# Performance work log

Measured on AMD Instinct MI355X. Metric: run time of the kernel, lower is better.

## Reference

```python
import jax, jax.numpy as jnp
import numpy as np

NUM_EXPERTS = 8
TOP_K = 2
N_EMBD = 1024
D_FFN = 2048  # 4*n_embd//top_k, already multiple of block_size=128


def setup_inputs() -> dict:
    key = jax.random.key(0)
    k1, k2, k3, k4 = jax.random.split(key, 4)
    x = jax.random.normal(k1, (4, 2048, N_EMBD), dtype=jnp.float32)
    router_w = jax.random.normal(k2, (NUM_EXPERTS, N_EMBD), dtype=jnp.float32) * 0.02
    w1 = jax.random.normal(k3, (N_EMBD, D_FFN * NUM_EXPERTS), dtype=jnp.float32) * 0.02
    w2 = jax.random.normal(k4, (D_FFN * NUM_EXPERTS, N_EMBD), dtype=jnp.float32) * 0.02
    return {"x": x, "router_w": router_w, "w1": w1, "w2": w2}


def reference(x, router_w, w1, w2):
    B, T, D = x.shape
    xf = x.reshape(B * T, D)                       # [N, d]
    N = B * T

    # Router: softmax over experts, then top-k selection and renormalization.
    logits = xf @ router_w.T                       # [N, E]
    probs = jax.nn.softmax(logits, axis=-1)
    top_v, top_i = jax.lax.top_k(probs, TOP_K)     # [N, k]
    top_v = top_v / jnp.sum(top_v, axis=-1, keepdims=True)  # norm_topk_prob=True

    # Dense [N, E] routing-weight matrix (zero for non-selected experts).
    gate = jnp.zeros((N, NUM_EXPERTS), dtype=x.dtype)
    gate = gate.at[jnp.arange(N)[:, None], top_i].set(top_v)

    w1r = w1.reshape(D, NUM_EXPERTS, D_FFN)        # expert-major column blocks
    w2r = w2.reshape(NUM_EXPERTS, D_FFN, D)

    out = jnp.zeros((N, D), dtype=x.dtype)
    for e in range(NUM_EXPERTS):
        h = jax.nn.gelu(xf @ w1r[:, e, :], approximate=False)  # [N, f]
        out = out + gate[:, e:e + 1] * (h @ w2r[e])
    return out.reshape(B, T, D)
```

## Files before the change

kernel.cpp:

```cpp
#include <hip/hip_runtime.h>
#include <hip/hip_bf16.h>
#include <cstdint>
#include <cstddef>

#define NE 8
#define N_TOK 8192
#define D_EMB 1024
#define D_FFN 2048

#define BM 128
#define BN 128
#define BK 32

typedef __attribute__((ext_vector_type(8))) short short8;
typedef __attribute__((ext_vector_type(4))) float f32x4;

__device__ __forceinline__ unsigned short f2bf(float f) {
  union { float f; unsigned int u; } c; c.f = f;
  unsigned int u = c.u;
  unsigned int r = u + 0x7FFFu + ((u >> 16) & 1u);
  return (unsigned short)(r >> 16);
}

__device__ __forceinline__ float bf2f(unsigned short u) {
  union { unsigned int u; float f; } c; c.u = ((unsigned int)u) << 16;
  return c.f;
}

__device__ __forceinline__ float gelu_f(float x) {
  float u = x * x * x * 0.044715f + x;
  float t = __expf(-1.5957691216057308f * u);
  return x * __builtin_amdgcn_rcpf(1.f + t);
}

__device__ __forceinline__ void gll16(const void* g, void* l) {
  __builtin_amdgcn_global_load_lds((const __attribute__((address_space(1))) void*)g,
                                   (__attribute__((address_space(3))) void*)l, 16, 0, 0);
}

#define SB() __builtin_amdgcn_sched_barrier(0)
#define VW(N) { asm volatile("s_waitcnt vmcnt(" #N ")" ::: "memory"); SB(); }
#define BAR() { SB(); __builtin_amdgcn_s_barrier(); SB(); }

__global__ __launch_bounds__(256) void router_k(const float* __restrict__ x,
                                                const float* __restrict__ rw,
                                                int* __restrict__ ti,
                                                float* __restrict__ tg,
                                                ushort* __restrict__ xb) {
  int w = threadIdx.x >> 6, lane = threadIdx.x & 63;
  int n = blockIdx.x * 4 + w;
  const float4* x4 = (const float4*)(x + (size_t)n * D_EMB);
  ushort4* xb4 = (ushort4*)(xb + (size_t)n * D_EMB);
  const float4* r4 = (const float4*)rw;
  float acc[NE];
#pragma unroll
  for (int e = 0; e < NE; ++e) acc[e] = 0.f;
#pragma unroll
  for (int c = 0; c < 4; ++c) {
    float4 xv = x4[c * 64 + lane];
    ushort4 o;
    o.x = f2bf(xv.x); o.y = f2bf(xv.y); o.z = f2bf(xv.z); o.w = f2bf(xv.w);
    xb4[c * 64 + lane] = o;
#pragma unroll
    for (int e = 0; e < NE; ++e) {
      float4 wv = r4[e * 256 + c * 64 + lane];
      acc[e] += xv.x * wv.x + xv.y * wv.y + xv.z * wv.z + xv.w * wv.w;
    }
  }
#pragma unroll
  for (int e = 0; e < NE; ++e) {
    float v = acc[e];
#pragma unroll
    for (int off = 32; off >= 1; off >>= 1) v += __shfl_xor(v, off);
    acc[e] = v;
  }
  if (lane == 0) {
    int e0 = 0; float v0 = acc[0];
#pragma unroll
    for (int e = 1; e < NE; ++e) if (acc[e] > v0) { v0 = acc[e]; e0 = e; }
    int e1 = -1; float v1 = -1e30f;
#pragma unroll
    for (int e = 0; e < NE; ++e) if (e != e0 && acc[e] > v1) { v1 = acc[e]; e1 = e; }
    float p1 = expf(v1 - v0);
    float g0 = 1.f / (1.f + p1);
    float g1 = p1 * g0;
    ti[2 * n] = e0; ti[2 * n + 1] = e1;
    tg[2 * n] = g0; tg[2 * n + 1] = g1;
  }
}

__global__ __launch_bounds__(256) void hist_k(const int* __restrict__ ti,
                                              int* __restrict__ counts) {
  __shared__ int lc[NE];
  if (threadIdx.x < NE) lc[threadIdx.x] = 0;
  __syncthreads();
  int s = blockIdx.x * 512 + threadIdx.x;
  atomicAdd(&lc[ti[s]], 1);
  atomicAdd(&lc[ti[s + 256]], 1);
  __syncthreads();
  if (threadIdx.x < NE) atomicAdd(&counts[threadIdx.x], lc[threadIdx.x]);
}

__global__ void prefix_k(const int* __restrict__ counts, int* __restrict__ bases,
                         int* __restrict__ cursor) {
  if (threadIdx.x == 0) {
    int s = 0;
    for (int e = 0; e < NE; ++e) { bases[e] = s; cursor[e] = s; s += counts[e]; }
  }
}

__global__ __launch_bounds__(256) void scatter_k(const int* __restrict__ ti,
                                                 const float* __restrict__ tg,
                                                 int* __restrict__ cursor,
                                                 int* __restrict__ tokS,
                                                 float* __restrict__ gate) {
  __shared__ int lc[NE], lb[NE];
  if (threadIdx.x < NE) lc[threadIdx.x] = 0;
  __syncthreads();
  int s = blockIdx.x * 256 + threadIdx.x;
  int e = ti[s];
  float g = tg[s];
  int loc = atomicAdd(&lc[e], 1);
  __syncthreads();
  if (threadIdx.x < NE) lb[threadIdx.x] = atomicAdd(&cursor[threadIdx.x], lc[threadIdx.x]);
  __syncthreads();
  int pos = lb[e] + loc;
  tokS[pos] = s;
  gate[pos] = g;
}

__global__ __launch_bounds__(256) void transpose_bf_k(const float* __restrict__ src,
                                                      ushort* __restrict__ dst,
                                                      int R, int C) {
  __shared__ ushort t[32][33];
  int bx = blockIdx.x, by = blockIdx.y;
  int rl = threadIdx.x >> 3, q = threadIdx.x & 7;
  float4 v = *(const float4*)&src[(size_t)(by * 32 + rl) * C + bx * 32 + q * 4];
  t[rl][q * 4 + 0] = f2bf(v.x);
  t[rl][q * 4 + 1] = f2bf(v.y);
  t[rl][q * 4 + 2] = f2bf(v.z);
  t[rl][q * 4 + 3] = f2bf(v.w);
  __syncthreads();
  ushort4 o;
  o.x = t[q * 4 + 0][rl];
  o.y = t[q * 4 + 1][rl];
  o.z = t[q * 4 + 2][rl];
  o.w = t[q * 4 + 3][rl];
  *(ushort4*)&dst[(size_t)(bx * 32 + rl) * R + by * 32 + q * 4] = o;
}

__global__ __launch_bounds__(256) void transpose_w2e_k(const float* __restrict__ src,
                                                       ushort* __restrict__ dst) {
  __shared__ ushort t[32][33];
  int bx = blockIdx.x, by = blockIdx.y;
  int rl = threadIdx.x >> 3, q = threadIdx.x & 7;
  float4 v = *(const float4*)&src[(size_t)(by * 32 + rl) * D_EMB + bx * 32 + q * 4];
  t[rl][q * 4 + 0] = f2bf(v.x);
  t[rl][q * 4 + 1] = f2bf(v.y);
  t[rl][q * 4 + 2] = f2bf(v.z);
  t[rl][q * 4 + 3] = f2bf(v.w);
  __syncthreads();
  int e = by >> 6;
  int f0 = (by & 63) * 32;
  size_t eoff = (size_t)e * (D_EMB * D_FFN);
  ushort4 o;
  o.x = t[q * 4 + 0][rl];
  o.y = t[q * 4 + 1][rl];
  o.z = t[q * 4 + 2][rl];
  o.w = t[q * 4 + 3][rl];
  *(ushort4*)&dst[eoff + (size_t)(bx * 32 + rl) * D_FFN + f0 + q * 4] = o;
}


#define STG(BUF)                                                           \
  { _Pragma("unroll") for (int j_ = 0; j_ < 2; ++j_) {                     \
      gll16(aptr[j_], &Al[BUF][ldso[j_]]);                                 \
      gll16(bptr[j_], &Bl[BUF][ldso[j_]]);                                 \
      aptr[j_] += BK; bptr[j_] += BK;                                      \
    } }

#define CMP(BUF)                                                           \
  { short8 a[4], b[4];                                                     \
    _Pragma("unroll") for (int i_ = 0; i_ < 4; ++i_)                       \
      a[i_] = *(const short8*)&Al[BUF][arow + i_ * 16 * BK];               \
    _Pragma("unroll") for (int j_ = 0; j_ < 4; ++j_)                       \
      b[j_] = *(const short8*)&Bl[BUF][brow + j_ * 16 * BK];               \
    _Pragma("unroll") for (int i_ = 0; i_ < 4; ++i_)                       \
      _Pragma("unroll") for (int j_ = 0; j_ < 4; ++j_)                     \
        acc[i_][j_] = __builtin_amdgcn_mfma_f32_16x16x32_bf16(a[i_], b[j_], acc[i_][j_], 0, 0, 0); \
  }

#define KLOOP(NT)                                                          \
  STG(0);                                                                  \
  for (int ks = 0; ks < (NT) - 2; ks += 2) {                               \
    STG(1); VW(4); BAR(); CMP(0); BAR();                                   \
    STG(0); VW(4); BAR(); CMP(1); BAR();                                   \
  }                                                                        \
  STG(1); VW(4); BAR(); CMP(0); BAR();                                     \
  VW(0); BAR(); CMP(1);

#define KLOOP3(NT)                                                         \
  STG(0); STG(1);                                                          \
  for (int ks = 0; ks < (NT) - 2; ks += 3) {                               \
    STG(2); VW(8); BAR(); CMP(0); BAR();                                   \
    STG(0); VW(8); BAR(); CMP(1); BAR();                                   \
    STG(1); VW(8); BAR(); CMP(2); BAR();                                   \
  }                                                                        \
  VW(4); BAR(); CMP(0); BAR();                                             \
  VW(0); BAR(); CMP(1);

__global__ __launch_bounds__(256) void gemm1_k(const ushort* __restrict__ xb,
                                               const ushort* __restrict__ w1t,
                                               const int* __restrict__ counts,
                                               const int* __restrict__ bases,
                                               const int* __restrict__ tokS,
                                               ushort* __restrict__ h) {
  int bid = (int)blockIdx.x;
  bid = (bid & 7) * (NE * 1024 / 8) + (bid >> 3);
  int e = bid >> 10;
  int rem = bid & 1023;
  int mt = rem >> 4, nt = rem & 15;
  int count = counts[e];
  if (mt * BM >= count) return;
  int base = bases[e];

  __shared__ ushort Al[3][BM * BK];
  __shared__ ushort Bl[3][BN * BK];

  int tid = threadIdx.x;
  int w = tid >> 6, lane = tid & 63;

  const int ssw = (((lane & 3) ^ ((lane >> 3) & 3))) * 8;

  const ushort* aptr[2]; const ushort* bptr[2];
  int ldso[2];
#pragma unroll
  for (int j = 0; j < 2; ++j) {
    int rl = w * 32 + j * 16 + (lane >> 2);
    int pr = min(base + mt * BM + rl, base + count - 1);
    int t = tokS[pr] >> 1;
    aptr[j] = xb + (size_t)t * D_EMB + ssw;
    int c = e * D_FFN + nt * BN + rl;
    bptr[j] = w1t + (size_t)c * D_EMB + ssw;
    ldso[j] = (w * 32 + j * 16) * BK;
  }

  f32x4 zero = {0.f, 0.f, 0.f, 0.f};
  f32x4 acc[4][4];
#pragma unroll
  for (int i = 0; i < 4; ++i)
#pragma unroll
    for (int j = 0; j < 4; ++j) acc[i][j] = zero;

  int wm = w >> 1, wn = w & 1;
  const int rsw = ((lane >> 4) ^ (((lane & 15) >> 1) & 3)) * 8;
  const int arow = (wm * 64 + (lane & 15)) * BK + rsw;
  const int brow = (wn * 64 + (lane & 15)) * BK + rsw;

  KLOOP3(D_EMB / BK);

  int r0 = mt * BM + wm * 64, c0 = nt * BN + wn * 64;
#pragma unroll
  for (int i = 0; i < 4; ++i) {
#pragma unroll
    for (int q = 0; q < 4; ++q) {
      int row = r0 + i * 16 + (lane >> 4) * 4 + q;
      if (row < count) {
        size_t hb = (size_t)(base + row) * D_FFN;
#pragma unroll
        for (int j = 0; j < 4; ++j) {
          h[hb + c0 + j * 16 + (lane & 15)] = f2bf(gelu_f(acc[i][j][q]));
        }
      }
    }
  }
}

__global__ __launch_bounds__(256) void gemm2_k(const ushort* __restrict__ h,
                                               const ushort* __restrict__ w2te,
                                               const int* __restrict__ counts,
                                               const int* __restrict__ bases,
                                               const int* __restrict__ tokS,
                                               const float* __restrict__ gate,
                                               ushort* __restrict__ y2) {
  int bid = (int)blockIdx.x;
  bid = (bid & 7) * (NE * 512 / 8) + (bid >> 3);
  int e = bid >> 9;
  int rem = bid & 511;
  int mt = rem >> 3, nt = rem & 7;
  int count = counts[e];
  if (mt * BM >= count) return;
  int base = bases[e];

  __shared__ ushort Al[2][BM * BK];
  __shared__ ushort Bl[2][BN * BK];

  int tid = threadIdx.x;
  int w = tid >> 6, lane = tid & 63;

  const int ssw = (((lane & 3) ^ ((lane >> 3) & 3))) * 8;

  const ushort* aptr[2]; const ushort* bptr[2];
  int ldso[2];
#pragma unroll
  for (int j = 0; j < 2; ++j) {
    int rl = w * 32 + j * 16 + (lane >> 2);
    int pr = min(base + mt * BM + rl, base + count - 1);
    aptr[j] = h + (size_t)pr * D_FFN + ssw;
    int d = nt * BN + rl;
    bptr[j] = w2te + (size_t)e * (D_EMB * D_FFN) + (size_t)d * D_FFN + ssw;
    ldso[j] = (w * 32 + j * 16) * BK;
  }

  f32x4 zero = {0.f, 0.f, 0.f, 0.f};
  f32x4 acc[4][4];
#pragma unroll
  for (int i = 0; i < 4; ++i)
#pragma unroll
    for (int j = 0; j < 4; ++j) acc[i][j] = zero;

  int wm = w >> 1, wn = w & 1;
  const int rsw = ((lane >> 4) ^ (((lane & 15) >> 1) & 3)) * 8;
  const int arow = (wm * 64 + (lane & 15)) * BK + rsw;
  const int brow = (wn * 64 + (lane & 15)) * BK + rsw;

  KLOOP(D_FFN / BK);

  int r0 = mt * BM + wm * 64, c0 = nt * BN + wn * 64;
#pragma unroll
  for (int i = 0; i < 4; ++i) {
#pragma unroll
    for (int q = 0; q < 4; ++q) {
      int row = r0 + i * 16 + (lane >> 4) * 4 + q;
      if (row < count) {
        int pr = base + row;
        float g = gate[pr];
        size_t yb = (size_t)tokS[pr] * D_EMB;
#pragma unroll
        for (int j = 0; j < 4; ++j) {
          y2[yb + c0 + j * 16 + (lane & 15)] = f2bf(g * acc[i][j][q]);
        }
      }
    }
  }
}

__global__ __launch_bounds__(256) void combine_k(const ushort* __restrict__ y2,
                                                 float* __restrict__ out) {
  int n = blockIdx.x;
  const ushort4* r0 = (const ushort4*)(y2 + (size_t)(2 * n) * D_EMB);
  const ushort4* r1 = (const ushort4*)(y2 + (size_t)(2 * n + 1) * D_EMB);
  float4* o = (float4*)(out + (size_t)n * D_EMB);
  int i = threadIdx.x;
  ushort4 a = r0[i], b = r1[i];
  float4 v;
  v.x = bf2f(a.x) + bf2f(b.x);
  v.y = bf2f(a.y) + bf2f(b.y);
  v.z = bf2f(a.z) + bf2f(b.z);
  v.w = bf2f(a.w) + bf2f(b.w);
  o[i] = v;
}

extern "C" void kernel_launch(void* const* d_in, const int* in_sizes, int n_in,
                              void* d_out, int out_size, void* d_ws, size_t ws_size,
                              hipStream_t stream) {
  const float* x  = (const float*)d_in[0];
  const float* rw = (const float*)d_in[1];
  const float* w1 = (const float*)d_in[2];
  const float* w2 = (const float*)d_in[3];
  float* out = (float*)d_out;

  char* ws = (char*)d_ws;
  size_t off = 0;
  auto alloc = [&](size_t bytes) {
    void* p = ws + off;
    off = (off + bytes + 255) & ~(size_t)255;
    return p;
  };
  int*    counts = (int*)alloc(32);
  int*    bases  = (int*)alloc(32);
  int*    cursor = (int*)alloc(32);
  int*    ti     = (int*)alloc((size_t)N_TOK * 2 * sizeof(int));
  float*  tg     = (float*)alloc((size_t)N_TOK * 2 * sizeof(float));
  int*    tokS   = (int*)alloc((size_t)N_TOK * 2 * sizeof(int));
  float*  gate   = (float*)alloc((size_t)N_TOK * 2 * sizeof(float));
  ushort* xb     = (ushort*)alloc((size_t)N_TOK * D_EMB * 2);
  ushort* w1t    = (ushort*)alloc((size_t)D_EMB * NE * D_FFN * 2);
  ushort* w2te   = (ushort*)alloc((size_t)D_EMB * NE * D_FFN * 2);
  ushort* hbuf   = (ushort*)alloc((size_t)N_TOK * 2 * D_FFN * 2);
  ushort* ybuf   = (ushort*)alloc((size_t)N_TOK * 2 * D_EMB * 2);
  (void)ws_size; (void)in_sizes; (void)n_in; (void)out_size;

  hipMemsetAsync(counts, 0, 32, stream);

  router_k<<<N_TOK / 4, 256, 0, stream>>>(x, rw, ti, tg, xb);
  transpose_bf_k<<<dim3(512, 32), 256, 0, stream>>>(w1, w1t, D_EMB, NE * D_FFN);
  transpose_w2e_k<<<dim3(32, 512), 256, 0, stream>>>(w2, w2te);
  hist_k<<<N_TOK * 2 / 512, 256, 0, stream>>>(ti, counts);
  prefix_k<<<1, 64, 0, stream>>>(counts, bases, cursor);
  scatter_k<<<N_TOK * 2 / 256, 256, 0, stream>>>(ti, tg, cursor, tokS, gate);
  gemm1_k<<<NE * 64 * 16, 256, 0, stream>>>(xb, w1t, counts, bases, tokS, hbuf);
  gemm2_k<<<NE * 64 * 8, 256, 0, stream>>>(hbuf, w2te, counts, bases, tokS, gate, ybuf);
  combine_k<<<N_TOK, 256, 0, stream>>>(ybuf, out);
}
```

Measured before the change: 307.6 us.

## Rewrite expert down-projection GEMM with 256x256 tiles and 8-wave blocks

The second expert GEMM moves from 128x128 tiles with BK=32 and 4 waves to 256x256 tiles with BK=64 and 8 waves. Each wave computes 128x64 of output. Operand tiles are double-buffered in 128KB of dynamic LDS with an XOR swizzle, and the global loads for the next tile are interleaved between sub-steps of the MFMA work. The aim is more data reuse per LDS load and fewer global loads of weights and activations per output element. The first GEMM also drops its triple-buffered K loop for the plain double-buffered one, which frees LDS but may expose more load latency. The large LDS footprint limits gemm2 to one block per CU, and the grid now wastes more rows on padded tail tiles.

```diff
diff --git a/kernel.cpp b/kernel.cpp
--- a/kernel.cpp
+++ b/kernel.cpp
@@ -197,16 +197,6 @@
     STG(0); VW(4); BAR(); CMP(1); BAR();                                   \
   }                                                                        \
   STG(1); VW(4); BAR(); CMP(0); BAR();                                     \
-  VW(0); BAR(); CMP(1);
-
-#define KLOOP3(NT)                                                         \
-  STG(0); STG(1);                                                          \
-  for (int ks = 0; ks < (NT) - 2; ks += 3) {                               \
-    STG(2); VW(8); BAR(); CMP(0); BAR();                                   \
-    STG(0); VW(8); BAR(); CMP(1); BAR();                                   \
-    STG(1); VW(8); BAR(); CMP(2); BAR();                                   \
-  }                                                                        \
-  VW(4); BAR(); CMP(0); BAR();                                             \
   VW(0); BAR(); CMP(1);
 
 __global__ __launch_bounds__(256) void gemm1_k(const ushort* __restrict__ xb,
@@ -224,8 +214,8 @@
   if (mt * BM >= count) return;
   int base = bases[e];
 
-  __shared__ ushort Al[3][BM * BK];
-  __shared__ ushort Bl[3][BN * BK];
+  __shared__ ushort Al[2][BM * BK];
+  __shared__ ushort Bl[2][BN * BK];
 
   int tid = threadIdx.x;
   int w = tid >> 6, lane = tid & 63;
@@ -257,7 +247,7 @@
   const int arow = (wm * 64 + (lane & 15)) * BK + rsw;
   const int brow = (wn * 64 + (lane & 15)) * BK + rsw;
 
-  KLOOP3(D_EMB / BK);
+  KLOOP(D_EMB / BK);
 
   int r0 = mt * BM + wm * 64, c0 = nt * BN + wn * 64;
 #pragma unroll
@@ -276,7 +266,57 @@
   }
 }
 
-__global__ __launch_bounds__(256) void gemm2_k(const ushort* __restrict__ h,
+
+#define SA2(ABUF)                                                          \
+  { _Pragma("unroll") for (int r_ = 0; r_ < 4; ++r_) {                     \
+      gll16(aP[r_], &(ABUF)[(r_ * 64 + (tid >> 3)) * 64 + (tid & 7) * 8]); \
+      aP[r_] += 64;                                                        \
+    } }
+
+#define SB2(BBUF)                                                          \
+  { _Pragma("unroll") for (int r_ = 0; r_ < 4; ++r_) {                     \
+      gll16(bP[r_], &(BBUF)[(r_ * 64 + (tid >> 3)) * 64 + (tid & 7) * 8]); \
+      bP[r_] += 64;                                                        \
+    } }
+
+#define RDA2(DST, ABUF, F0)                                                \
+  { _Pragma("unroll") for (int f_ = 0; f_ < 4; ++f_) {                     \
+      DST[f_][0] = *(const short8*)&(ABUF)[(wm * 128 + ((F0) + f_) * 16 + l15) * 64 + q0];         \
+      DST[f_][1] = *(const short8*)&(ABUF)[(wm * 128 + ((F0) + f_) * 16 + l15) * 64 + (q0 ^ 32)];  \
+    } }
+
+#define RDB2(DST, BBUF, G0)                                                \
+  { _Pragma("unroll") for (int g_ = 0; g_ < 2; ++g_) {                     \
+      DST[g_][0] = *(const short8*)&(BBUF)[(wn * 64 + ((G0) + g_) * 16 + l15) * 64 + q0];          \
+      DST[g_][1] = *(const short8*)&(BBUF)[(wn * 64 + ((G0) + g_) * 16 + l15) * 64 + (q0 ^ 32)];   \
+    } }
+
+#define QMM(FA, FB, F0, G0)                                                \
+  { _Pragma("unroll") for (int f_ = 0; f_ < 4; ++f_)                       \
+    _Pragma("unroll") for (int g_ = 0; g_ < 2; ++g_)                       \
+    _Pragma("unroll") for (int k_ = 0; k_ < 2; ++k_)                       \
+      acc[(F0) + f_][(G0) + g_] = __builtin_amdgcn_mfma_f32_16x16x32_bf16( \
+          FA[f_][k_], FB[g_][k_], acc[(F0) + f_][(G0) + g_], 0, 0, 0);     \
+  }
+
+#define T256(CA, CB, NA, NB, DOS)                                          \
+  { if (DOS) { SA2(NA); VW(4); } else { VW(0); }                           \
+    BAR();                                                                 \
+    RDA2(fa, CA, 0); RDB2(fb, CB, 0);                                      \
+    QMM(fa, fb, 0, 0);                                                     \
+    BAR();                                                                 \
+    if (DOS) { SB2(NB); }                                                  \
+    RDB2(fb2, CB, 2);                                                      \
+    QMM(fa, fb2, 0, 2);                                                    \
+    BAR();                                                                 \
+    RDA2(fa, CA, 4);                                                       \
+    QMM(fa, fb2, 4, 2);                                                    \
+    BAR();                                                                 \
+    RDB2(fb, CB, 0);                                                       \
+    QMM(fa, fb, 4, 0);                                                     \
+    BAR(); }
+
+__global__ __launch_bounds__(512) void gemm2_k(const ushort* __restrict__ h,
                                                const ushort* __restrict__ w2te,
                                                const int* __restrict__ counts,
                                                const int* __restrict__ bases,
@@ -284,61 +324,69 @@
                                                const float* __restrict__ gate,
                                                ushort* __restrict__ y2) {
   int bid = (int)blockIdx.x;
-  bid = (bid & 7) * (NE * 512 / 8) + (bid >> 3);
-  int e = bid >> 9;
-  int rem = bid & 511;
-  int mt = rem >> 3, nt = rem & 7;
+  bid = (bid & 7) * 256 + (bid >> 3);
+  int e = bid >> 8;
+  int rem = bid & 255;
+  int mt = rem >> 2, nt = rem & 3;
   int count = counts[e];
-  if (mt * BM >= count) return;
+  if (mt * 256 >= count) return;
   int base = bases[e];
 
-  __shared__ ushort Al[2][BM * BK];
-  __shared__ ushort Bl[2][BN * BK];
+  extern __shared__ ushort smem[];
+  ushort* A0_ = smem;
+  ushort* A1_ = smem + 16384;
+  ushort* B0_ = smem + 32768;
+  ushort* B1_ = smem + 49152;
 
   int tid = threadIdx.x;
-  int w = tid >> 6, lane = tid & 63;
-
-  const int ssw = (((lane & 3) ^ ((lane >> 3) & 3))) * 8;
-
-  const ushort* aptr[2]; const ushort* bptr[2];
-  int ldso[2];
-#pragma unroll
-  for (int j = 0; j < 2; ++j) {
-    int rl = w * 32 + j * 16 + (lane >> 2);
-    int pr = min(base + mt * BM + rl, base + count - 1);
-    aptr[j] = h + (size_t)pr * D_FFN + ssw;
-    int d = nt * BN + rl;
-    bptr[j] = w2te + (size_t)e * (D_EMB * D_FFN) + (size_t)d * D_FFN + ssw;
-    ldso[j] = (w * 32 + j * 16) * BK;
+  int wv = tid >> 6, lane = tid & 63;
+  int wm = wv >> 2, wn = wv & 3;
+  const int l15 = lane & 15;
+  const int q0 = ((lane >> 4) ^ (lane & 7)) * 8;
+  const int swc = (((tid & 7) ^ ((tid >> 3) & 7))) * 8;
+
+  const ushort* aP[4]; const ushort* bP[4];
+#pragma unroll
+  for (int r = 0; r < 4; ++r) {
+    int R = r * 64 + (tid >> 3);
+    int pr = min(base + mt * 256 + R, base + count - 1);
+    aP[r] = h + (size_t)pr * D_FFN + swc;
+    int d = nt * 256 + R;
+    bP[r] = w2te + (size_t)e * (D_EMB * D_FFN) + (size_t)d * D_FFN + swc;
   }
 
   f32x4 zero = {0.f, 0.f, 0.f, 0.f};
-  f32x4 acc[4][4];
-#pragma unroll
-  for (int i = 0; i < 4; ++i)
+  f32x4 acc[8][4];
+#pragma unroll
+  for (int i = 0; i < 8; ++i)
 #pragma unroll
     for (int j = 0; j < 4; ++j) acc[i][j] = zero;
 
-  int wm = w >> 1, wn = w & 1;
-  const int rsw = ((lane >> 4) ^ (((lane & 15) >> 1) & 3)) * 8;
-  const int arow = (wm * 64 + (lane & 15)) * BK + rsw;
-  const int brow = (wn * 64 + (lane & 15)) * BK + rsw;
-
-  KLOOP(D_FFN / BK);
-
-  int r0 = mt * BM + wm * 64, c0 = nt * BN + wn * 64;
-#pragma unroll
-  for (int i = 0; i < 4; ++i) {
+  short8 fa[4][2], fb[2][2], fb2[2][2];
+
+  SA2(A0_); SB2(B0_);
+
+  const int NT = D_FFN / 64;
+  for (int tp = 0; tp < NT / 2 - 1; ++tp) {
+    T256(A0_, B0_, A1_, B1_, 1);
+    T256(A1_, B1_, A0_, B0_, 1);
+  }
+  T256(A0_, B0_, A1_, B1_, 1);
+  T256(A1_, B1_, A0_, B0_, 0);
+
+  int r0 = mt * 256 + wm * 128, c0 = nt * 256 + wn * 64;
+#pragma unroll
+  for (int f = 0; f < 8; ++f) {
 #pragma unroll
     for (int q = 0; q < 4; ++q) {
-      int row = r0 + i * 16 + (lane >> 4) * 4 + q;
+      int row = r0 + f * 16 + (lane >> 4) * 4 + q;
       if (row < count) {
         int pr = base + row;
         float g = gate[pr];
         size_t yb = (size_t)tokS[pr] * D_EMB;
 #pragma unroll
-        for (int j = 0; j < 4; ++j) {
-          y2[yb + c0 + j * 16 + (lane & 15)] = f2bf(g * acc[i][j][q]);
+        for (int g_ = 0; g_ < 4; ++g_) {
+          y2[yb + c0 + g_ * 16 + l15] = f2bf(g * acc[f][g_][q]);
         }
       }
     }
@@ -391,6 +439,8 @@
   ushort* ybuf   = (ushort*)alloc((size_t)N_TOK * 2 * D_EMB * 2);
   (void)ws_size; (void)in_sizes; (void)n_in; (void)out_size;
 
+  hipFuncSetAttribute((const void*)gemm2_k, hipFuncAttributeMaxDynamicSharedMemorySize, 131072);
+
   hipMemsetAsync(counts, 0, 32, stream);
 
   router_k<<<N_TOK / 4, 256, 0, stream>>>(x, rw, ti, tg, xb);
@@ -400,6 +450,6 @@
   prefix_k<<<1, 64, 0, stream>>>(counts, bases, cursor);
   scatter_k<<<N_TOK * 2 / 256, 256, 0, stream>>>(ti, tg, cursor, tokS, gate);
   gemm1_k<<<NE * 64 * 16, 256, 0, stream>>>(xb, w1t, counts, bases, tokS, hbuf);
-  gemm2_k<<<NE * 64 * 8, 256, 0, stream>>>(hbuf, w2te, counts, bases, tokS, gate, ybuf);
+  gemm2_k<<<NE * 64 * 4, 512, 131072, stream>>>(hbuf, w2te, counts, bases, tokS, gate, ybuf);
   combine_k<<<N_TOK, 256, 0, stream>>>(ybuf, out);
 }
```

Result: faster. 291.4 us (-5.2%).
